# Performance work log

Hardware: AMD Instinct MI355X
Metric: run time of the kernel (lower is better)

The kernel has to match this reference:

```python
import jax, jax.numpy as jnp
import numpy as np
from jax import lax

DIM = 256
KS = 7
EPS = 1e-6


def setup_inputs() -> dict:
    key = jax.random.key(0)
    ks = jax.random.split(key, 10)
    x = jax.random.normal(ks[0], (32, DIM, 56, 56), dtype=jnp.float32)
    mask = jax.random.randint(ks[1], (32, 1, 7, 7), 0, 2, dtype=jnp.int32)
    dw_w = jax.random.normal(ks[2], (DIM, 1, KS, KS), dtype=jnp.float32) * (1.0 / KS)
    dw_b = jax.random.normal(ks[3], (DIM,), dtype=jnp.float32) * 0.01
    ln_w = jnp.ones((DIM,), dtype=jnp.float32)
    ln_b = jnp.zeros((DIM,), dtype=jnp.float32)
    w1 = jax.random.normal(ks[4], (DIM, 4 * DIM), dtype=jnp.float32) * (1.0 / np.sqrt(DIM))
    b1 = jax.random.normal(ks[5], (4 * DIM,), dtype=jnp.float32) * 0.01
    w2 = jax.random.normal(ks[6], (4 * DIM, DIM), dtype=jnp.float32) * (1.0 / np.sqrt(4 * DIM))
    b2 = jax.random.normal(ks[7], (DIM,), dtype=jnp.float32) * 0.01
    gamma = jnp.full((DIM,), 1e-6, dtype=jnp.float32)
    return {"x": x, "mask": mask, "dw_w": dw_w, "dw_b": dw_b, "ln_w": ln_w,
            "ln_b": ln_b, "w1": w1, "b1": b1, "w2": w2, "b2": b2, "gamma": gamma}


def _expand_mask(mask, H, W):
    # repeat_interleave the (B,1,f,f) mask up to (B,1,H,W)
    hr, wr = H // mask.shape[-2], W // mask.shape[-1]
    m = jnp.repeat(jnp.repeat(mask, hr, axis=2), wr, axis=3)
    return m


def reference(x, mask, dw_w, dw_b, ln_w, ln_b, w1, b1, w2, b2, gamma):
    B, C, H, W = x.shape
    m = _expand_mask(mask, H, W).astype(x.dtype)  # (B,1,H,W)
    inp = x
    # depthwise conv, 'same' padding
    pad = KS // 2
    y = lax.conv_general_dilated(
        x, dw_w, window_strides=(1, 1), padding=[(pad, pad), (pad, pad)],
        feature_group_count=C, dimension_numbers=("NCHW", "OIHW", "NCHW"))
    y = y + dw_b[None, :, None, None]
    y = y.transpose(0, 2, 3, 1)  # (B,H,W,C)
    # sparse LayerNorm: gather-norm-scatter == per-position LN zeroed at inactive
    mu = jnp.mean(y, axis=-1, keepdims=True)
    var = jnp.mean((y - mu) ** 2, axis=-1, keepdims=True)
    y = ((y - mu) * lax.rsqrt(var + EPS)) * ln_w + ln_b
    y = y * m[:, 0, :, :, None]
    # MLP
    h = jax.nn.gelu(jnp.einsum("bhwc,cd->bhwd", y, w1) + b1, approximate=False)
    z = (jnp.einsum("bhwd,dc->bhwc", h, w2) + b2) * gamma
    z = z.transpose(0, 3, 1, 2)  # (B,C,H,W)
    z = z * m
    return inp + z
```

## Files before the change

### kernel.cpp

```cpp
#include <hip/hip_runtime.h>
#include <math.h>

#define HW   56
#define DIMC 256
#define HID  1024

typedef __attribute__((ext_vector_type(8))) short bf16x8;
typedef __attribute__((ext_vector_type(4))) float f32x4;

__device__ __forceinline__ short f2bf(float f) {
  union { float fv; unsigned u; } v; v.fv = f;
  unsigned r = v.u + 0x7fffu + ((v.u >> 16) & 1u);
  return (short)(r >> 16);
}
__device__ __forceinline__ float bf2f(short s) {
  union { unsigned u; float fv; } v; v.u = ((unsigned)(unsigned short)s) << 16;
  return v.fv;
}
__device__ __forceinline__ float gelu_fast(float v) {
  float e = exp2f(-2.4556260f * v);
  return v * __builtin_amdgcn_rcpf(1.f + e);
}
__device__ __forceinline__ long pk8(float f0, float f1, float f2, float f3,
                                    float f4, float f5, float f6, float f7) {
  int lo = __builtin_amdgcn_cvt_pk_fp8_f32(f0, f1, 0, false);
  lo = __builtin_amdgcn_cvt_pk_fp8_f32(f2, f3, lo, true);
  int hi = __builtin_amdgcn_cvt_pk_fp8_f32(f4, f5, 0, false);
  hi = __builtin_amdgcn_cvt_pk_fp8_f32(f6, f7, hi, true);
  return ((long)(unsigned)lo) | ((long)hi << 32);
}
__device__ __forceinline__ char f2fp8(float f) {
  return (char)(__builtin_amdgcn_cvt_pk_fp8_f32(f, f, 0, false) & 0xff);
}

__global__ void prep_pack(const float* __restrict__ w1, const float* __restrict__ w2,
                          long* __restrict__ w1p, long* __restrict__ w2p) {
  int g = blockIdx.x * 256 + threadIdx.x;
  int f = g >> 6, lane = g & 63;
  int l15 = lane & 15, q = lane >> 4;
  float t[8];
  if (f < 512) {
    int k8 = f & 7, tt = f >> 3, nt = tt & 1, ch = tt >> 1;
    int n = ch * 32 + nt * 16 + l15;
    int k = k8 * 32 + q * 8;
    #pragma unroll
    for (int j = 0; j < 8; ++j) t[j] = w1[(k + j) * HID + n];
    w1p[f * 64 + lane] = pk8(t[0], t[1], t[2], t[3], t[4], t[5], t[6], t[7]);
  } else {
    int f2 = f - 512;
    int nt2 = f2 & 15, ch = f2 >> 4;
    int k = ch * 32 + q * 8;
    int c = nt2 * 16 + l15;
    #pragma unroll
    for (int j = 0; j < 8; ++j) t[j] = w2[(k + j) * DIMC + c];
    w2p[f2 * 64 + lane] = pk8(t[0], t[1], t[2], t[3], t[4], t[5], t[6], t[7]);
  }
}

__global__ __launch_bounds__(256, 3) void conv_k(
    const float* __restrict__ x, const int* __restrict__ mask,
    const float* __restrict__ dw_w, const float* __restrict__ dw_b,
    short* __restrict__ ybuf) {
  __shared__ __align__(16) float s_patch[32 * 14 * 20];
  __shared__ float s_wt[32 * 49];
  __shared__ __align__(16) short s_yout[32 * 64];

  int bid = blockIdx.x;
  int cgi = bid & 7; int t1 = bid >> 3;
  int wb = t1 % 7; int t2 = t1 / 7; int hb = t2 % 7; int b = t2 / 7;
  int tile = (b * 7 + hb) * 7 + wb;
  if (!mask[tile]) return;

  int tid = threadIdx.x;
  int h0 = hb * 8, w0 = wb * 8, cg0 = cgi * 32;

  for (int i = tid; i < 32 * 49; i += 256) s_wt[i] = dw_w[cg0 * 49 + i];

  #pragma unroll
  for (int it = 0; it < 7; ++it) {
    int slot = tid + 256 * it;
    int j = slot & 3, row = slot >> 2;
    int c = row / 14, r = row - c * 14;
    int gh = h0 - 3 + r;
    f32x4 v = (f32x4){0.f, 0.f, 0.f, 0.f};
    bool ok = (gh >= 0) && (gh < HW) && !(wb == 0 && j == 0) && !(wb == 6 && j == 3);
    if (ok)
      v = *(const f32x4*)(x + ((long)(b * DIMC + cg0 + c) * HW + gh) * HW + (w0 - 4) + 4 * j);
    *(f32x4*)(s_patch + c * 280 + r * 20 + 4 * j) = v;
  }
  __syncthreads();

  int cl = tid >> 3, wq = tid & 7;
  float wt[49];
  #pragma unroll
  for (int j = 0; j < 49; ++j) wt[j] = s_wt[cl * 49 + j];
  float y[8] = {0.f, 0.f, 0.f, 0.f, 0.f, 0.f, 0.f, 0.f};
  #pragma unroll
  for (int r = 0; r < 14; ++r) {
    float row[7];
    #pragma unroll
    for (int j = 0; j < 7; ++j) row[j] = s_patch[cl * 280 + r * 20 + wq + 1 + j];
    #pragma unroll
    for (int dy = 0; dy < 7; ++dy) {
      int hh = r - dy;
      if (hh >= 0 && hh < 8) {
        #pragma unroll
        for (int dx = 0; dx < 7; ++dx) y[hh] += row[dx] * wt[dy * 7 + dx];
      }
    }
  }
  float db = dw_b[cg0 + cl];
  #pragma unroll
  for (int hh = 0; hh < 8; ++hh)
    s_yout[cl * 64 + hh * 8 + wq] = f2bf(y[hh] + db);
  __syncthreads();

  int c = tid >> 3, pd = (tid & 7) * 8;
  bf16x8 v = *(const bf16x8*)(s_yout + c * 64 + pd);
  *(bf16x8*)(ybuf + ((long)tile * DIMC + cg0 + c) * 64 + pd) = v;
}

__global__ __launch_bounds__(256, 3) void mlp_k(
    const int* __restrict__ mask,
    const float* __restrict__ ln_w, const float* __restrict__ ln_b,
    const float* __restrict__ b1v, const float* __restrict__ b2v,
    const float* __restrict__ gammav,
    const long* __restrict__ w1p, const long* __restrict__ w2p,
    short* __restrict__ ybuf) {
  __shared__ __align__(16) char smem[46592];
  short* s_a   = (short*)smem;
  short* s_del = (short*)smem;
  char*  s_h8  = smem + 36864;
  float* s_p1  = (float*)(smem + 41984);
  float* s_p2  = (float*)(smem + 43008);
  float* s_mu  = (float*)(smem + 44032);
  float* s_rs  = (float*)(smem + 44288);
  float* s_lnw = (float*)(smem + 44544);
  float* s_lnb = (float*)(smem + 45568);

  int tile = blockIdx.x;
  if (!mask[tile]) return;
  int tid = threadIdx.x;
  const short* ytile = ybuf + (long)tile * DIMC * 64;

  s_lnw[tid] = ln_w[tid];
  s_lnb[tid] = ln_b[tid];
  #pragma unroll
  for (int k = 0; k < 8; ++k) {
    int q4 = tid + 256 * k;
    int c = q4 & 255, pd = (q4 >> 8) * 8;
    bf16x8 v = *(const bf16x8*)(ytile + c * 64 + pd);
    #pragma unroll
    for (int j = 0; j < 8; ++j) s_a[(pd + j) * 264 + c] = v[j];
  }
  __syncthreads();

  {
    int p = tid & 63, cq = tid >> 6;
    bf16x8 va[8];
    float s1 = 0.f, s2 = 0.f;
    #pragma unroll
    for (int i = 0; i < 8; ++i) {
      va[i] = *(const bf16x8*)(s_a + p * 264 + cq * 64 + i * 8);
      #pragma unroll
      for (int j = 0; j < 8; ++j) {
        float f = bf2f(va[i][j]);
        s1 += f; s2 += f * f;
      }
    }
    s_p1[cq * 64 + p] = s1; s_p2[cq * 64 + p] = s2;
    __syncthreads();
    if (tid < 64) {
      float t1 = s_p1[tid] + s_p1[64 + tid] + s_p1[128 + tid] + s_p1[192 + tid];
      float t2 = s_p2[tid] + s_p2[64 + tid] + s_p2[128 + tid] + s_p2[192 + tid];
      float mu = t1 * (1.f / 256.f);
      float var = t2 * (1.f / 256.f) - mu * mu;
      s_mu[tid] = mu; s_rs[tid] = rsqrtf(var + 1e-6f);
    }
    __syncthreads();
    float mu = s_mu[p], rs = s_rs[p];
    #pragma unroll
    for (int i = 0; i < 8; ++i) {
      int c0 = cq * 64 + i * 8;
      bf16x8 v = va[i];
      #pragma unroll
      for (int j = 0; j < 8; ++j)
        v[j] = f2bf((bf2f(v[j]) - mu) * rs * s_lnw[c0 + j] + s_lnb[c0 + j]);
      *(bf16x8*)(s_a + p * 264 + c0) = v;
    }
  }
  __syncthreads();

  const int wv = tid >> 6, lane = tid & 63;
  const int l15 = lane & 15, q = lane >> 4;
  const int mh = wv & 1, nh = wv >> 1;

  const short* aRow0 = s_a + (32 * mh + l15) * 264 + q * 8;
  const short* aRow1 = s_a + (32 * mh + 16 + l15) * 264 + q * 8;
  long a0f[8], a1f[8];
  #pragma unroll
  for (int k8 = 0; k8 < 8; ++k8) {
    bf16x8 v0 = *(const bf16x8*)(aRow0 + k8 * 32);
    bf16x8 v1 = *(const bf16x8*)(aRow1 + k8 * 32);
    a0f[k8] = pk8(bf2f(v0[0]), bf2f(v0[1]), bf2f(v0[2]), bf2f(v0[3]),
                  bf2f(v0[4]), bf2f(v0[5]), bf2f(v0[6]), bf2f(v0[7]));
    a1f[k8] = pk8(bf2f(v1[0]), bf2f(v1[1]), bf2f(v1[2]), bf2f(v1[3]),
                  bf2f(v1[4]), bf2f(v1[5]), bf2f(v1[6]), bf2f(v1[7]));
  }

  f32x4 z[4][4];
  #pragma unroll
  for (int jt = 0; jt < 4; ++jt)
    #pragma unroll
    for (int Mt = 0; Mt < 4; ++Mt) z[jt][Mt] = (f32x4){0.f, 0.f, 0.f, 0.f};

  long w1r[8];
  #pragma unroll
  for (int k8 = 0; k8 < 8; ++k8)
    w1r[k8] = w1p[(long)(nh * 8 + k8) * 64 + lane];

  for (int ch = 0; ch < 32; ++ch) {
    long w2r[4];
    #pragma unroll
    for (int jt = 0; jt < 4; ++jt)
      w2r[jt] = w2p[(long)(ch * 16 + wv * 4 + jt) * 64 + lane];
    float bb = b1v[ch * 32 + 16 * nh + l15];

    f32x4 acc0 = (f32x4){0.f, 0.f, 0.f, 0.f};
    f32x4 acc1 = (f32x4){0.f, 0.f, 0.f, 0.f};
    __builtin_amdgcn_s_setprio(1);
    #pragma unroll
    for (int k8 = 0; k8 < 8; ++k8) {
      acc0 = __builtin_amdgcn_mfma_f32_16x16x32_fp8_fp8(a0f[k8], w1r[k8], acc0, 0, 0, 0);
      acc1 = __builtin_amdgcn_mfma_f32_16x16x32_fp8_fp8(a1f[k8], w1r[k8], acc1, 0, 0, 0);
    }
    __builtin_amdgcn_s_setprio(0);
    long w1n[8];
    if (ch < 31) {
      #pragma unroll
      for (int k8 = 0; k8 < 8; ++k8)
        w1n[k8] = w1p[(long)(((ch + 1) * 2 + nh) * 8 + k8) * 64 + lane];
    }
    char* hb = s_h8 + (ch & 1) * 2560;
    #pragma unroll
    for (int r = 0; r < 4; ++r) {
      hb[(32 * mh + 4 * q + r) * 40 + 16 * nh + l15]      = f2fp8(gelu_fast(acc0[r] + bb));
      hb[(32 * mh + 16 + 4 * q + r) * 40 + 16 * nh + l15] = f2fp8(gelu_fast(acc1[r] + bb));
    }
    __syncthreads();
    __builtin_amdgcn_s_setprio(1);
    #pragma unroll
    for (int Mt = 0; Mt < 4; ++Mt) {
      long aH = *(const long*)(hb + (16 * Mt + l15) * 40 + q * 8);
      #pragma unroll
      for (int jt = 0; jt < 4; ++jt)
        z[jt][Mt] = __builtin_amdgcn_mfma_f32_16x16x32_fp8_fp8(aH, w2r[jt], z[jt][Mt], 0, 0, 0);
    }
    __builtin_amdgcn_s_setprio(0);
    if (ch < 31) {
      #pragma unroll
      for (int k8 = 0; k8 < 8; ++k8) w1r[k8] = w1n[k8];
    }
  }

  #pragma unroll
  for (int jt = 0; jt < 4; ++jt) {
    int c = wv * 64 + jt * 16 + l15;
    float bb = b2v[c], gm = gammav[c];
    #pragma unroll
    for (int Mt = 0; Mt < 4; ++Mt) {
      #pragma unroll
      for (int r = 0; r < 4; ++r)
        s_del[c * 72 + 16 * Mt + 4 * q + r] = f2bf((z[jt][Mt][r] + bb) * gm);
    }
  }
  __syncthreads();
  short* dtile = ybuf + (long)tile * DIMC * 64;
  #pragma unroll
  for (int k = 0; k < 8; ++k) {
    int q4 = tid + 256 * k;
    int c = q4 & 255, pd = (q4 >> 8) * 8;
    bf16x8 v = *(const bf16x8*)(s_del + c * 72 + pd);
    *(bf16x8*)(dtile + c * 64 + pd) = v;
  }
}

__global__ __launch_bounds__(256) void epi_k(
    const float* __restrict__ x, const int* __restrict__ mask,
    const short* __restrict__ delta, float* __restrict__ out) {
  const int NU = 32 * DIMC * HW * 7;
  int stride = gridDim.x * 256;
  for (int u = blockIdx.x * 256 + threadIdx.x; u < NU; u += stride) {
    int wb = u % 7; int t1 = u / 7;
    int h = t1 % 56; int t2 = t1 / 56;
    int c = t2 & 255; int b = t2 >> 8;
    int g = ((b * DIMC + c) * HW + h) * HW + wb * 8;
    f32x4 x0 = *(const f32x4*)(x + g);
    f32x4 x1 = *(const f32x4*)(x + g + 4);
    int tile = (b * 7 + (h >> 3)) * 7 + wb;
    if (mask[tile]) {
      bf16x8 d = *(const bf16x8*)(delta + ((long)tile * DIMC + c) * 64 + (h & 7) * 8);
      #pragma unroll
      for (int i = 0; i < 4; ++i) { x0[i] += bf2f(d[i]); x1[i] += bf2f(d[4 + i]); }
    }
    *(f32x4*)(out + g) = x0;
    *(f32x4*)(out + g + 4) = x1;
  }
}

extern "C" void kernel_launch(void* const* d_in, const int* in_sizes, int n_in,
                              void* d_out, int out_size, void* d_ws, size_t ws_size,
                              hipStream_t stream) {
  const float* x    = (const float*)d_in[0];
  const int*   mask = (const int*)d_in[1];
  const float* dw_w = (const float*)d_in[2];
  const float* dw_b = (const float*)d_in[3];
  const float* ln_w = (const float*)d_in[4];
  const float* ln_b = (const float*)d_in[5];
  const float* w1   = (const float*)d_in[6];
  const float* b1   = (const float*)d_in[7];
  const float* w2   = (const float*)d_in[8];
  const float* b2   = (const float*)d_in[9];
  const float* gm   = (const float*)d_in[10];
  float* out = (float*)d_out;

  long* w1p  = (long*)d_ws;
  long* w2p  = w1p + 512 * 64;
  short* ybuf = (short*)(w2p + 512 * 64);

  prep_pack<<<256, 256, 0, stream>>>(w1, w2, w1p, w2p);
  conv_k<<<12544, 256, 0, stream>>>(x, mask, dw_w, dw_b, ybuf);
  mlp_k<<<1568, 256, 0, stream>>>(mask, ln_w, ln_b, b1, b2, gm, w1p, w2p, ybuf);
  epi_k<<<4096, 256, 0, stream>>>(x, mask, ybuf, out);
}
```

Measured before the change: 372.7 us.

## Compact active tiles into a list and use persistent work-queue conv and MLP kernels

A new kernel builds a compacted list of active mask tiles with an atomic counter. The conv and MLP kernels become persistent grids that pull work items from atomic queues, so they no longer launch and immediately retire blocks for masked-out tiles. Conv also switches to 16-channel work units with 4-row halves per thread, reads weights directly from global memory, and raises the occupancy hint. In exchange it adds an extra launch, serialised atomics, and per-item barrier overhead in the persistent loops.

Measured after the change: 443.6 us. 19.0% more time.

```diff
diff --git a/kernel.cpp b/kernel.cpp
--- a/kernel.cpp
+++ b/kernel.cpp
@@ -34,8 +34,10 @@
 }
 
 __global__ void prep_pack(const float* __restrict__ w1, const float* __restrict__ w2,
-                          long* __restrict__ w1p, long* __restrict__ w2p) {
+                          long* __restrict__ w1p, long* __restrict__ w2p,
+                          int* __restrict__ qmeta) {
   int g = blockIdx.x * 256 + threadIdx.x;
+  if (g == 0) { qmeta[0] = 0; qmeta[1] = 0; qmeta[2] = 0; }
   int f = g >> 6, lane = g & 63;
   int l15 = lane & 15, q = lane >> 4;
   float t[8];
@@ -57,77 +59,95 @@
   }
 }
 
-__global__ __launch_bounds__(256, 3) void conv_k(
-    const float* __restrict__ x, const int* __restrict__ mask,
-    const float* __restrict__ dw_w, const float* __restrict__ dw_b,
+__global__ void compact_k(const int* __restrict__ mask, int* __restrict__ qmeta) {
+  int t = blockIdx.x * 256 + threadIdx.x;
+  if (t < 1568 && mask[t]) {
+    int i = atomicAdd(qmeta, 1);
+    qmeta[16 + i] = t;
+  }
+}
+
+__global__ __launch_bounds__(256, 4) void conv_k(
+    const float* __restrict__ x, const float* __restrict__ dw_w,
+    const float* __restrict__ dw_b, int* __restrict__ qmeta,
     short* __restrict__ ybuf) {
-  __shared__ __align__(16) float s_patch[32 * 14 * 20];
-  __shared__ float s_wt[32 * 49];
-  __shared__ __align__(16) short s_yout[32 * 64];
-
-  int bid = blockIdx.x;
-  int cgi = bid & 7; int t1 = bid >> 3;
-  int wb = t1 % 7; int t2 = t1 / 7; int hb = t2 % 7; int b = t2 / 7;
-  int tile = (b * 7 + hb) * 7 + wb;
-  if (!mask[tile]) return;
-
+  __shared__ __align__(16) float s_patch[16 * 14 * 20];
+  __shared__ int s_u;
+  short* s_yout = (short*)s_patch;
+  const int* list = qmeta + 16;
   int tid = threadIdx.x;
-  int h0 = hb * 8, w0 = wb * 8, cg0 = cgi * 32;
-
-  for (int i = tid; i < 32 * 49; i += 256) s_wt[i] = dw_w[cg0 * 49 + i];
-
-  #pragma unroll
-  for (int it = 0; it < 7; ++it) {
-    int slot = tid + 256 * it;
-    int j = slot & 3, row = slot >> 2;
-    int c = row / 14, r = row - c * 14;
-    int gh = h0 - 3 + r;
-    f32x4 v = (f32x4){0.f, 0.f, 0.f, 0.f};
-    bool ok = (gh >= 0) && (gh < HW) && !(wb == 0 && j == 0) && !(wb == 6 && j == 3);
-    if (ok)
-      v = *(const f32x4*)(x + ((long)(b * DIMC + cg0 + c) * HW + gh) * HW + (w0 - 4) + 4 * j);
-    *(f32x4*)(s_patch + c * 280 + r * 20 + 4 * j) = v;
-  }
-  __syncthreads();
-
-  int cl = tid >> 3, wq = tid & 7;
-  float wt[49];
-  #pragma unroll
-  for (int j = 0; j < 49; ++j) wt[j] = s_wt[cl * 49 + j];
-  float y[8] = {0.f, 0.f, 0.f, 0.f, 0.f, 0.f, 0.f, 0.f};
-  #pragma unroll
-  for (int r = 0; r < 14; ++r) {
-    float row[7];
-    #pragma unroll
-    for (int j = 0; j < 7; ++j) row[j] = s_patch[cl * 280 + r * 20 + wq + 1 + j];
-    #pragma unroll
-    for (int dy = 0; dy < 7; ++dy) {
-      int hh = r - dy;
-      if (hh >= 0 && hh < 8) {
-        #pragma unroll
-        for (int dx = 0; dx < 7; ++dx) y[hh] += row[dx] * wt[dy * 7 + dx];
-      }
-    }
-  }
-  float db = dw_b[cg0 + cl];
-  #pragma unroll
-  for (int hh = 0; hh < 8; ++hh)
-    s_yout[cl * 64 + hh * 8 + wq] = f2bf(y[hh] + db);
-  __syncthreads();
-
-  int c = tid >> 3, pd = (tid & 7) * 8;
-  bf16x8 v = *(const bf16x8*)(s_yout + c * 64 + pd);
-  *(bf16x8*)(ybuf + ((long)tile * DIMC + cg0 + c) * 64 + pd) = v;
+  int total = qmeta[0] * 16;
+
+  for (;;) {
+    if (tid == 0) s_u = atomicAdd(qmeta + 2, 1);
+    __syncthreads();
+    int u = s_u;
+    if (u >= total) break;
+    int tile = list[u >> 4], cgi = u & 15;
+    int wb = tile % 7; int t2 = tile / 7; int hb = t2 % 7; int b = t2 / 7;
+    int h0 = hb * 8, w0 = wb * 8, cg0 = cgi * 16;
+
+    #pragma unroll
+    for (int it = 0; it < 4; ++it) {
+      int slot = tid + 256 * it;
+      if (slot < 896) {
+        int j = slot & 3, row = slot >> 2;
+        int c = row / 14, r = row - c * 14;
+        int gh = h0 - 3 + r;
+        f32x4 v = (f32x4){0.f, 0.f, 0.f, 0.f};
+        bool ok = (gh >= 0) && (gh < HW) && !(wb == 0 && j == 0) && !(wb == 6 && j == 3);
+        if (ok)
+          v = *(const f32x4*)(x + ((long)(b * DIMC + cg0 + c) * HW + gh) * HW + (w0 - 4) + 4 * j);
+        *(f32x4*)(s_patch + c * 280 + r * 20 + 4 * j) = v;
+      }
+    }
+
+    int cl = tid >> 4, s = tid & 15;
+    int wq = s & 7, hf = s >> 3;
+    float wt[49];
+    #pragma unroll
+    for (int j = 0; j < 49; ++j) wt[j] = dw_w[(cg0 + cl) * 49 + j];
+    __syncthreads();
+
+    float y[4] = {0.f, 0.f, 0.f, 0.f};
+    #pragma unroll
+    for (int rr = 0; rr < 10; ++rr) {
+      float row[7];
+      #pragma unroll
+      for (int j = 0; j < 7; ++j) row[j] = s_patch[cl * 280 + (hf * 4 + rr) * 20 + wq + 1 + j];
+      #pragma unroll
+      for (int dy = 0; dy < 7; ++dy) {
+        int hh = rr - dy;
+        if (hh >= 0 && hh < 4) {
+          #pragma unroll
+          for (int dx = 0; dx < 7; ++dx) y[hh] += row[dx] * wt[dy * 7 + dx];
+        }
+      }
+    }
+    float db = dw_b[cg0 + cl];
+    __syncthreads();
+    #pragma unroll
+    for (int hh = 0; hh < 4; ++hh)
+      s_yout[cl * 64 + (hf * 4 + hh) * 8 + wq] = f2bf(y[hh] + db);
+    __syncthreads();
+
+    if (tid < 128) {
+      int c = tid >> 3, pd = (tid & 7) * 8;
+      bf16x8 v = *(const bf16x8*)(s_yout + c * 64 + pd);
+      *(bf16x8*)(ybuf + ((long)tile * DIMC + cg0 + c) * 64 + pd) = v;
+    }
+    __syncthreads();
+  }
 }
 
 __global__ __launch_bounds__(256, 3) void mlp_k(
-    const int* __restrict__ mask,
     const float* __restrict__ ln_w, const float* __restrict__ ln_b,
     const float* __restrict__ b1v, const float* __restrict__ b2v,
     const float* __restrict__ gammav,
     const long* __restrict__ w1p, const long* __restrict__ w2p,
-    short* __restrict__ ybuf) {
+    int* __restrict__ qmeta, short* __restrict__ ybuf) {
   __shared__ __align__(16) char smem[46592];
+  __shared__ int s_u;
   short* s_a   = (short*)smem;
   short* s_del = (short*)smem;
   char*  s_h8  = smem + 36864;
@@ -138,150 +158,159 @@
   float* s_lnw = (float*)(smem + 44544);
   float* s_lnb = (float*)(smem + 45568);
 
-  int tile = blockIdx.x;
-  if (!mask[tile]) return;
+  const int* list = qmeta + 16;
   int tid = threadIdx.x;
-  const short* ytile = ybuf + (long)tile * DIMC * 64;
+  int total = qmeta[0];
 
   s_lnw[tid] = ln_w[tid];
   s_lnb[tid] = ln_b[tid];
-  #pragma unroll
-  for (int k = 0; k < 8; ++k) {
-    int q4 = tid + 256 * k;
-    int c = q4 & 255, pd = (q4 >> 8) * 8;
-    bf16x8 v = *(const bf16x8*)(ytile + c * 64 + pd);
-    #pragma unroll
-    for (int j = 0; j < 8; ++j) s_a[(pd + j) * 264 + c] = v[j];
-  }
-  __syncthreads();
-
-  {
-    int p = tid & 63, cq = tid >> 6;
-    bf16x8 va[8];
-    float s1 = 0.f, s2 = 0.f;
-    #pragma unroll
-    for (int i = 0; i < 8; ++i) {
-      va[i] = *(const bf16x8*)(s_a + p * 264 + cq * 64 + i * 8);
-      #pragma unroll
-      for (int j = 0; j < 8; ++j) {
-        float f = bf2f(va[i][j]);
-        s1 += f; s2 += f * f;
-      }
-    }
-    s_p1[cq * 64 + p] = s1; s_p2[cq * 64 + p] = s2;
-    __syncthreads();
-    if (tid < 64) {
-      float t1 = s_p1[tid] + s_p1[64 + tid] + s_p1[128 + tid] + s_p1[192 + tid];
-      float t2 = s_p2[tid] + s_p2[64 + tid] + s_p2[128 + tid] + s_p2[192 + tid];
-      float mu = t1 * (1.f / 256.f);
-      float var = t2 * (1.f / 256.f) - mu * mu;
-      s_mu[tid] = mu; s_rs[tid] = rsqrtf(var + 1e-6f);
-    }
-    __syncthreads();
-    float mu = s_mu[p], rs = s_rs[p];
-    #pragma unroll
-    for (int i = 0; i < 8; ++i) {
-      int c0 = cq * 64 + i * 8;
-      bf16x8 v = va[i];
-      #pragma unroll
-      for (int j = 0; j < 8; ++j)
-        v[j] = f2bf((bf2f(v[j]) - mu) * rs * s_lnw[c0 + j] + s_lnb[c0 + j]);
-      *(bf16x8*)(s_a + p * 264 + c0) = v;
-    }
-  }
-  __syncthreads();
 
   const int wv = tid >> 6, lane = tid & 63;
   const int l15 = lane & 15, q = lane >> 4;
   const int mh = wv & 1, nh = wv >> 1;
 
-  const short* aRow0 = s_a + (32 * mh + l15) * 264 + q * 8;
-  const short* aRow1 = s_a + (32 * mh + 16 + l15) * 264 + q * 8;
-  long a0f[8], a1f[8];
-  #pragma unroll
-  for (int k8 = 0; k8 < 8; ++k8) {
-    bf16x8 v0 = *(const bf16x8*)(aRow0 + k8 * 32);
-    bf16x8 v1 = *(const bf16x8*)(aRow1 + k8 * 32);
-    a0f[k8] = pk8(bf2f(v0[0]), bf2f(v0[1]), bf2f(v0[2]), bf2f(v0[3]),
-                  bf2f(v0[4]), bf2f(v0[5]), bf2f(v0[6]), bf2f(v0[7]));
-    a1f[k8] = pk8(bf2f(v1[0]), bf2f(v1[1]), bf2f(v1[2]), bf2f(v1[3]),
-                  bf2f(v1[4]), bf2f(v1[5]), bf2f(v1[6]), bf2f(v1[7]));
-  }
-
-  f32x4 z[4][4];
-  #pragma unroll
-  for (int jt = 0; jt < 4; ++jt)
-    #pragma unroll
-    for (int Mt = 0; Mt < 4; ++Mt) z[jt][Mt] = (f32x4){0.f, 0.f, 0.f, 0.f};
-
-  long w1r[8];
-  #pragma unroll
-  for (int k8 = 0; k8 < 8; ++k8)
-    w1r[k8] = w1p[(long)(nh * 8 + k8) * 64 + lane];
-
-  for (int ch = 0; ch < 32; ++ch) {
-    long w2r[4];
+  for (;;) {
+    if (tid == 0) s_u = atomicAdd(qmeta + 1, 1);
+    __syncthreads();
+    int i = s_u;
+    if (i >= total) break;
+    int tile = list[i];
+    short* ytile = ybuf + (long)tile * DIMC * 64;
+
+    #pragma unroll
+    for (int k = 0; k < 8; ++k) {
+      int q4 = tid + 256 * k;
+      int c = q4 & 255, pd = (q4 >> 8) * 8;
+      bf16x8 v = *(const bf16x8*)(ytile + c * 64 + pd);
+      #pragma unroll
+      for (int j = 0; j < 8; ++j) s_a[(pd + j) * 264 + c] = v[j];
+    }
+    __syncthreads();
+
+    {
+      int p = tid & 63, cq = tid >> 6;
+      bf16x8 va[8];
+      float s1 = 0.f, s2 = 0.f;
+      #pragma unroll
+      for (int ii = 0; ii < 8; ++ii) {
+        va[ii] = *(const bf16x8*)(s_a + p * 264 + cq * 64 + ii * 8);
+        #pragma unroll
+        for (int j = 0; j < 8; ++j) {
+          float f = bf2f(va[ii][j]);
+          s1 += f; s2 += f * f;
+        }
+      }
+      s_p1[cq * 64 + p] = s1; s_p2[cq * 64 + p] = s2;
+      __syncthreads();
+      if (tid < 64) {
+        float t1 = s_p1[tid] + s_p1[64 + tid] + s_p1[128 + tid] + s_p1[192 + tid];
+        float t2 = s_p2[tid] + s_p2[64 + tid] + s_p2[128 + tid] + s_p2[192 + tid];
+        float mu = t1 * (1.f / 256.f);
+        float var = t2 * (1.f / 256.f) - mu * mu;
+        s_mu[tid] = mu; s_rs[tid] = rsqrtf(var + 1e-6f);
+      }
+      __syncthreads();
+      float mu = s_mu[p], rs = s_rs[p];
+      #pragma unroll
+      for (int ii = 0; ii < 8; ++ii) {
+        int c0 = cq * 64 + ii * 8;
+        bf16x8 v = va[ii];
+        #pragma unroll
+        for (int j = 0; j < 8; ++j)
+          v[j] = f2bf((bf2f(v[j]) - mu) * rs * s_lnw[c0 + j] + s_lnb[c0 + j]);
+        *(bf16x8*)(s_a + p * 264 + c0) = v;
+      }
+    }
+    __syncthreads();
+
+    const short* aRow0 = s_a + (32 * mh + l15) * 264 + q * 8;
+    const short* aRow1 = s_a + (32 * mh + 16 + l15) * 264 + q * 8;
+    long a0f[8], a1f[8];
+    #pragma unroll
+    for (int k8 = 0; k8 < 8; ++k8) {
+      bf16x8 v0 = *(const bf16x8*)(aRow0 + k8 * 32);
+      bf16x8 v1 = *(const bf16x8*)(aRow1 + k8 * 32);
+      a0f[k8] = pk8(bf2f(v0[0]), bf2f(v0[1]), bf2f(v0[2]), bf2f(v0[3]),
+                    bf2f(v0[4]), bf2f(v0[5]), bf2f(v0[6]), bf2f(v0[7]));
+      a1f[k8] = pk8(bf2f(v1[0]), bf2f(v1[1]), bf2f(v1[2]), bf2f(v1[3]),
+                    bf2f(v1[4]), bf2f(v1[5]), bf2f(v1[6]), bf2f(v1[7]));
+    }
+
+    f32x4 z[4][4];
     #pragma unroll
     for (int jt = 0; jt < 4; ++jt)
-      w2r[jt] = w2p[(long)(ch * 16 + wv * 4 + jt) * 64 + lane];
-    float bb = b1v[ch * 32 + 16 * nh + l15];
-
-    f32x4 acc0 = (f32x4){0.f, 0.f, 0.f, 0.f};
-    f32x4 acc1 = (f32x4){0.f, 0.f, 0.f, 0.f};
-    __builtin_amdgcn_s_setprio(1);
-    #pragma unroll
-    for (int k8 = 0; k8 < 8; ++k8) {
-      acc0 = __builtin_amdgcn_mfma_f32_16x16x32_fp8_fp8(a0f[k8], w1r[k8], acc0, 0, 0, 0);
-      acc1 = __builtin_amdgcn_mfma_f32_16x16x32_fp8_fp8(a1f[k8], w1r[k8], acc1, 0, 0, 0);
-    }
-    __builtin_amdgcn_s_setprio(0);
-    long w1n[8];
-    if (ch < 31) {
-      #pragma unroll
-      for (int k8 = 0; k8 < 8; ++k8)
-        w1n[k8] = w1p[(long)(((ch + 1) * 2 + nh) * 8 + k8) * 64 + lane];
-    }
-    char* hb = s_h8 + (ch & 1) * 2560;
-    #pragma unroll
-    for (int r = 0; r < 4; ++r) {
-      hb[(32 * mh + 4 * q + r) * 40 + 16 * nh + l15]      = f2fp8(gelu_fast(acc0[r] + bb));
-      hb[(32 * mh + 16 + 4 * q + r) * 40 + 16 * nh + l15] = f2fp8(gelu_fast(acc1[r] + bb));
-    }
-    __syncthreads();
-    __builtin_amdgcn_s_setprio(1);
-    #pragma unroll
-    for (int Mt = 0; Mt < 4; ++Mt) {
-      long aH = *(const long*)(hb + (16 * Mt + l15) * 40 + q * 8);
+      #pragma unroll
+      for (int Mt = 0; Mt < 4; ++Mt) z[jt][Mt] = (f32x4){0.f, 0.f, 0.f, 0.f};
+
+    long w1r[8];
+    #pragma unroll
+    for (int k8 = 0; k8 < 8; ++k8)
+      w1r[k8] = w1p[(long)(nh * 8 + k8) * 64 + lane];
+
+    for (int ch = 0; ch < 32; ++ch) {
+      long w2r[4];
       #pragma unroll
       for (int jt = 0; jt < 4; ++jt)
-        z[jt][Mt] = __builtin_amdgcn_mfma_f32_16x16x32_fp8_fp8(aH, w2r[jt], z[jt][Mt], 0, 0, 0);
-    }
-    __builtin_amdgcn_s_setprio(0);
-    if (ch < 31) {
-      #pragma unroll
-      for (int k8 = 0; k8 < 8; ++k8) w1r[k8] = w1n[k8];
-    }
-  }
-
-  #pragma unroll
-  for (int jt = 0; jt < 4; ++jt) {
-    int c = wv * 64 + jt * 16 + l15;
-    float bb = b2v[c], gm = gammav[c];
-    #pragma unroll
-    for (int Mt = 0; Mt < 4; ++Mt) {
-      #pragma unroll
-      for (int r = 0; r < 4; ++r)
-        s_del[c * 72 + 16 * Mt + 4 * q + r] = f2bf((z[jt][Mt][r] + bb) * gm);
-    }
-  }
-  __syncthreads();
-  short* dtile = ybuf + (long)tile * DIMC * 64;
-  #pragma unroll
-  for (int k = 0; k < 8; ++k) {
-    int q4 = tid + 256 * k;
-    int c = q4 & 255, pd = (q4 >> 8) * 8;
-    bf16x8 v = *(const bf16x8*)(s_del + c * 72 + pd);
-    *(bf16x8*)(dtile + c * 64 + pd) = v;
+        w2r[jt] = w2p[(long)(ch * 16 + wv * 4 + jt) * 64 + lane];
+      float bb = b1v[ch * 32 + 16 * nh + l15];
+
+      f32x4 acc0 = (f32x4){0.f, 0.f, 0.f, 0.f};
+      f32x4 acc1 = (f32x4){0.f, 0.f, 0.f, 0.f};
+      __builtin_amdgcn_s_setprio(1);
+      #pragma unroll
+      for (int k8 = 0; k8 < 8; ++k8) {
+        acc0 = __builtin_amdgcn_mfma_f32_16x16x32_fp8_fp8(a0f[k8], w1r[k8], acc0, 0, 0, 0);
+        acc1 = __builtin_amdgcn_mfma_f32_16x16x32_fp8_fp8(a1f[k8], w1r[k8], acc1, 0, 0, 0);
+      }
+      __builtin_amdgcn_s_setprio(0);
+      long w1n[8];
+      if (ch < 31) {
+        #pragma unroll
+        for (int k8 = 0; k8 < 8; ++k8)
+          w1n[k8] = w1p[(long)(((ch + 1) * 2 + nh) * 8 + k8) * 64 + lane];
+      }
+      char* hb = s_h8 + (ch & 1) * 2560;
+      #pragma unroll
+      for (int r = 0; r < 4; ++r) {
+        hb[(32 * mh + 4 * q + r) * 40 + 16 * nh + l15]      = f2fp8(gelu_fast(acc0[r] + bb));
+        hb[(32 * mh + 16 + 4 * q + r) * 40 + 16 * nh + l15] = f2fp8(gelu_fast(acc1[r] + bb));
+      }
+      __syncthreads();
+      __builtin_amdgcn_s_setprio(1);
+      #pragma unroll
+      for (int Mt = 0; Mt < 4; ++Mt) {
+        long aH = *(const long*)(hb + (16 * Mt + l15) * 40 + q * 8);
+        #pragma unroll
+        for (int jt = 0; jt < 4; ++jt)
+          z[jt][Mt] = __builtin_amdgcn_mfma_f32_16x16x32_fp8_fp8(aH, w2r[jt], z[jt][Mt], 0, 0, 0);
+      }
+      __builtin_amdgcn_s_setprio(0);
+      if (ch < 31) {
+        #pragma unroll
+        for (int k8 = 0; k8 < 8; ++k8) w1r[k8] = w1n[k8];
+      }
+    }
+
+    #pragma unroll
+    for (int jt = 0; jt < 4; ++jt) {
+      int c = wv * 64 + jt * 16 + l15;
+      float bb = b2v[c], gm = gammav[c];
+      #pragma unroll
+      for (int Mt = 0; Mt < 4; ++Mt) {
+        #pragma unroll
+        for (int r = 0; r < 4; ++r)
+          s_del[c * 72 + 16 * Mt + 4 * q + r] = f2bf((z[jt][Mt][r] + bb) * gm);
+      }
+    }
+    __syncthreads();
+    #pragma unroll
+    for (int k = 0; k < 8; ++k) {
+      int q4 = tid + 256 * k;
+      int c = q4 & 255, pd = (q4 >> 8) * 8;
+      bf16x8 v = *(const bf16x8*)(s_del + c * 72 + pd);
+      *(bf16x8*)(ytile + c * 64 + pd) = v;
+    }
+    __syncthreads();
   }
 }
 
@@ -326,10 +355,12 @@
 
   long* w1p  = (long*)d_ws;
   long* w2p  = w1p + 512 * 64;
-  short* ybuf = (short*)(w2p + 512 * 64);
-
-  prep_pack<<<256, 256, 0, stream>>>(w1, w2, w1p, w2p);
-  conv_k<<<12544, 256, 0, stream>>>(x, mask, dw_w, dw_b, ybuf);
-  mlp_k<<<1568, 256, 0, stream>>>(mask, ln_w, ln_b, b1, b2, gm, w1p, w2p, ybuf);
+  int*  qmeta = (int*)(w2p + 512 * 64);
+  short* ybuf = (short*)((char*)qmeta + 8192);
+
+  prep_pack<<<256, 256, 0, stream>>>(w1, w2, w1p, w2p, qmeta);
+  compact_k<<<7, 256, 0, stream>>>(mask, qmeta);
+  conv_k<<<1024, 256, 0, stream>>>(x, dw_w, dw_b, qmeta, ybuf);
+  mlp_k<<<768, 256, 0, stream>>>(ln_w, ln_b, b1, b2, gm, w1p, w2p, qmeta, ybuf);
   epi_k<<<4096, 256, 0, stream>>>(x, mask, ybuf, out);
 }
```
